# Kernel tuning notes

Measured on AMD Instinct MI355X. Metric: run time of the kernel, lower is better.

Reference implementation:

```python
import jax, jax.numpy as jnp
import numpy as np

# dims derived from config (hidden=512, d_state=64, d_conv=4, expand=2, headdim=64, ngroups=1)
D_MODEL = 512
D_STATE = 64
D_CONV = 4
D_INNER = 2 * D_MODEL          # 1024
HEADDIM = 64
NHEADS = D_INNER // HEADDIM    # 16
CONV_DIM = D_INNER + 2 * D_STATE   # 1152
D_IN_PROJ = 2 * D_INNER + 2 * D_STATE + NHEADS  # 2192
B = 4
L_TOT = 1024                   # seq_len (1008) + puzzle_emb_len (16)
INTER_T = 2816                 # find_multiple(round(4*1024*2/3), 256)
INTER_M = 1536                 # find_multiple(round(4*512*2/3), 256)
EPS = 1e-5


def rms_norm(x, eps=EPS):
    # weightless RMSNorm computed in fp32 (as HRM's rms_norm)
    x32 = x.astype(jnp.float32)
    y = x32 * jax.lax.rsqrt(jnp.mean(x32 * x32, axis=-1, keepdims=True) + eps)
    return y.astype(x.dtype)


def silu(x):
    return x * jax.nn.sigmoid(x)


def swiglu(x, w_gu, w_d):
    gate, up = jnp.split(x @ w_gu.T, 2, axis=-1)
    return (silu(gate) * up) @ w_d.T


def mamba2(u, in_proj_w, conv_w, conv_b, dt_bias, A_log, D, norm_w, out_proj_w):
    b, l, _ = u.shape
    zxbcdt = u @ in_proj_w.T                       # (b, l, D_IN_PROJ)
    z = zxbcdt[..., :D_INNER]
    xBC = zxbcdt[..., D_INNER:D_INNER + CONV_DIM]
    dt = jax.nn.softplus(zxbcdt[..., -NHEADS:] + dt_bias)  # (b, l, H)
    # causal depthwise conv1d over time + SiLU
    xp = jnp.pad(xBC, ((0, 0), (D_CONV - 1, 0), (0, 0)))
    xc = conv_b + sum(xp[:, i:i + l, :] * conv_w[:, i] for i in range(D_CONV))
    xBC = silu(xc)
    x = xBC[..., :D_INNER].reshape(b, l, NHEADS, HEADDIM)      # (b,l,h,p)
    Bm = xBC[..., D_INNER:D_INNER + D_STATE]                    # (b,l,n) ngroups=1
    Cm = xBC[..., D_INNER + D_STATE:]                           # (b,l,n)
    A = -jnp.exp(A_log)                                         # (h,)

    def step(s, inp):
        x_t, B_t, C_t, dt_t = inp                # (b,h,p) (b,n) (b,n) (b,h)
        dA = jnp.exp(dt_t * A)                   # (b,h)
        s = s * dA[:, :, None, None] + (dt_t[:, :, None] * x_t)[..., None] * B_t[:, None, None, :]
        y_t = jnp.einsum('bhpn,bn->bhp', s, C_t)
        return s, y_t

    s0 = jnp.zeros((b, NHEADS, HEADDIM, D_STATE), u.dtype)
    xs = (x.transpose(1, 0, 2, 3), Bm.transpose(1, 0, 2), Cm.transpose(1, 0, 2), dt.transpose(1, 0, 2))
    _, ys = jax.lax.scan(step, s0, xs)
    y = ys.transpose(1, 0, 2, 3) + x * D[None, None, :, None]   # skip term D*x per head
    y = y.reshape(b, l, D_INNER)
    # gated RMSNorm (norm_before_gate=False): norm(y * silu(z)) * weight
    g = y * silu(z)
    g32 = g.astype(jnp.float32)
    g = (g32 * jax.lax.rsqrt(jnp.mean(g32 * g32, axis=-1, keepdims=True) + EPS)).astype(g.dtype) * norm_w
    return g @ out_proj_w.T


def setup_inputs() -> dict:
    key = jax.random.key(0)
    ks = jax.random.split(key, 12)
    s = 0.02
    return {
        'hidden_states': jax.random.normal(ks[0], (B, L_TOT, D_MODEL), jnp.float32),
        'in_proj_w': jax.random.normal(ks[1], (D_IN_PROJ, D_MODEL), jnp.float32) * s,
        'conv_w': jax.random.normal(ks[2], (CONV_DIM, D_CONV), jnp.float32) * 0.1,
        'conv_b': jnp.zeros((CONV_DIM,), jnp.float32),
        'dt_bias': jax.random.normal(ks[3], (NHEADS,), jnp.float32) * 0.5,
        'A_log': jnp.log(jnp.arange(1, NHEADS + 1, dtype=jnp.float32)),
        'D': jnp.ones((NHEADS,), jnp.float32),
        'norm_w': jnp.ones((D_INNER,), jnp.float32),
        'out_proj_w': jax.random.normal(ks[4], (D_MODEL, D_INNER), jnp.float32) * s,
        'gu_t': jax.random.normal(ks[5], (2 * INTER_T, L_TOT), jnp.float32) * s,
        'down_t': jax.random.normal(ks[6], (L_TOT, INTER_T), jnp.float32) * s,
        'gu_m': jax.random.normal(ks[7], (2 * INTER_M, D_MODEL), jnp.float32) * s,
        'down_m': jax.random.normal(ks[8], (D_MODEL, INTER_M), jnp.float32) * s,
    }


def reference(hidden_states, in_proj_w, conv_w, conv_b, dt_bias, A_log, D, norm_w, out_proj_w, gu_t, down_t, gu_m, down_m):
    # Mamba2 mixer -> post-norm
    h = rms_norm(hidden_states + mamba2(hidden_states, in_proj_w, conv_w, conv_b, dt_bias, A_log, D, norm_w, out_proj_w))
    # MLP-t cross mixer over the sequence dim -> post-norm
    x = h.transpose(0, 2, 1)                 # (b, d, L)
    x = rms_norm(x + swiglu(x, gu_t, down_t))
    h = x.transpose(0, 2, 1)
    # token MLP -> post-norm
    h = rms_norm(h + swiglu(h, gu_m, down_m))
    return h
```

## Files before the change

### kernel.cpp

```cpp
#include <hip/hip_runtime.h>


#define BB 4
#define LL 1024
#define DMODEL 512
#define DINNER 1024
#define NHEADS 16
#define HEADDIM 64
#define DSTATE 64
#define CONVDIM 1152
#define NPROJ 2192
#define NPROJ_PAD 2304
#define INTER_T 2816
#define INTER_M 1536
#define NCHUNK 32
#define CHUNK 32

typedef __bf16 bf16x8 __attribute__((ext_vector_type(8)));
typedef float  f32x4  __attribute__((ext_vector_type(4)));
typedef unsigned short u16;
typedef unsigned int   u32;

__device__ __forceinline__ u16 f2bf(float x) {
    union { float f; u32 u; } v; v.f = x;
    u32 u = v.u;
    return (u16)((u + 0x7fffu + ((u >> 16) & 1u)) >> 16);
}
__device__ __forceinline__ float silu_f(float x) {
    return x / (1.f + __expf(-x));
}
__device__ __forceinline__ float bf2f(u16 w) {
    union { u32 u; float f; } a; a.u = ((u32)w) << 16; return a.f;
}

__device__ __forceinline__ void gld_lds16(const u16* g, u16* l) {
    __builtin_amdgcn_global_load_lds(
        (const __attribute__((address_space(1))) unsigned int*)g,
        (__attribute__((address_space(3))) unsigned int*)l, 16, 0, 0);
}

__device__ __forceinline__ float block_sum(float v) {
    #pragma unroll
    for (int off = 32; off > 0; off >>= 1) v += __shfl_xor(v, off, 64);
    __shared__ float red[4];
    int w = threadIdx.x >> 6;
    int nwv = blockDim.x >> 6;
    if ((threadIdx.x & 63) == 0) red[w] = v;
    __syncthreads();
    float tot = red[0];
    for (int i = 1; i < nwv; i++) tot += red[i];
    return tot;
}

#define HID_E      2097152LL
#define INPROJ_P_E 1179648LL
#define INPROJ_S_E 1122304LL
#define OUTPROJ_E   524288LL
#define GUT_E      5767168LL
#define DOWNT_E    2883584LL
#define GUM_E      1572864LL
#define DOWNM_E     786432LL
#define CONV_TOT_E 14811136LL

__global__ __launch_bounds__(256) void convert_all_kernel(
    const float* __restrict__ s_hid, const float* __restrict__ s_inproj,
    const float* __restrict__ s_outproj, const float* __restrict__ s_gut,
    const float* __restrict__ s_downt, const float* __restrict__ s_gum,
    const float* __restrict__ s_downm, u16* __restrict__ dst)
{
    long long idx = (long long)blockIdx.x * 256 + threadIdx.x;
    long long e = idx * 4;
    if (e >= CONV_TOT_E) return;
    const float* src; long long off, nsrc;
    long long c0 = HID_E;
    long long c1 = c0 + INPROJ_P_E;
    long long c2 = c1 + OUTPROJ_E;
    long long c3 = c2 + GUT_E;
    long long c4 = c3 + DOWNT_E;
    long long c5 = c4 + GUM_E;
    if      (e < c0) { src = s_hid;     off = e;      nsrc = HID_E; }
    else if (e < c1) { src = s_inproj;  off = e - c0; nsrc = INPROJ_S_E; }
    else if (e < c2) { src = s_outproj; off = e - c1; nsrc = OUTPROJ_E; }
    else if (e < c3) { src = s_gut;     off = e - c2; nsrc = GUT_E; }
    else if (e < c4) { src = s_downt;   off = e - c3; nsrc = DOWNT_E; }
    else if (e < c5) { src = s_gum;     off = e - c4; nsrc = GUM_E; }
    else             { src = s_downm;   off = e - c5; nsrc = DOWNM_E; }
    ushort4 r;
    if (off < nsrc) {
        float4 v = *reinterpret_cast<const float4*>(src + off);
        r.x = f2bf(v.x); r.y = f2bf(v.y); r.z = f2bf(v.z); r.w = f2bf(v.w);
    } else {
        r.x = 0; r.y = 0; r.z = 0; r.w = 0;
    }
    *reinterpret_cast<ushort4*>(dst + e) = r;
}

template<bool SK>
__device__ __forceinline__ void gemm_bt_body(
    const u16* __restrict__ A, const u16* __restrict__ W,
    float* __restrict__ C, int M, int N, int K, int kLen)
{
    __shared__ u16 As[128 * 64];
    __shared__ u16 Bs[128 * 64];
    int tid = threadIdx.x;
    int m0 = blockIdx.y * 128, n0 = blockIdx.x * 128;
    int kBase = SK ? blockIdx.z * kLen : 0;
    float* Cw = SK ? C + (size_t)blockIdx.z * M * N : C;
    int wave = tid >> 6, lane = tid & 63;
    int wm = (wave >> 1) * 64, wn = (wave & 1) * 64;
    int lrow = lane & 15;
    int kq = lane >> 4;
    int kx = lrow & 7;

    int rL = lane >> 3, cL = lane & 7;
    int cG = cL ^ rL;
    const u16* gA[4]; const u16* gB[4];
    u16 *lA[4], *lB[4];
    #pragma unroll
    for (int i = 0; i < 4; i++) {
        int r = wave * 32 + i * 8;
        gA[i] = A + (size_t)(m0 + r + rL) * K + kBase + cG * 8;
        gB[i] = W + (size_t)(n0 + r + rL) * K + kBase + cG * 8;
        lA[i] = &As[r * 64];
        lB[i] = &Bs[r * 64];
    }

    f32x4 acc[4][4];
    #pragma unroll
    for (int i = 0; i < 4; i++)
        #pragma unroll
        for (int j = 0; j < 4; j++) {
            acc[i][j][0] = 0.f; acc[i][j][1] = 0.f;
            acc[i][j][2] = 0.f; acc[i][j][3] = 0.f;
        }

    for (int kt = 0; kt < kLen; kt += 64) {
        __syncthreads();
        #pragma unroll
        for (int i = 0; i < 4; i++) {
            gld_lds16(gA[i] + kt, lA[i]);
            gld_lds16(gB[i] + kt, lB[i]);
        }
        __syncthreads();
        #pragma unroll
        for (int ks = 0; ks < 2; ks++) {
            int ko = (((ks * 4 + kq) ^ kx) * 8);
            bf16x8 af[4], bfr[4];
            #pragma unroll
            for (int i = 0; i < 4; i++) {
                af[i]  = *reinterpret_cast<const bf16x8*>(&As[(wm + i * 16 + lrow) * 64 + ko]);
                bfr[i] = *reinterpret_cast<const bf16x8*>(&Bs[(wn + i * 16 + lrow) * 64 + ko]);
            }
            #pragma unroll
            for (int i = 0; i < 4; i++)
                #pragma unroll
                for (int j = 0; j < 4; j++)
                    acc[i][j] = __builtin_amdgcn_mfma_f32_16x16x32_bf16(af[i], bfr[j], acc[i][j], 0, 0, 0);
        }
    }

    int rbase = m0 + wm + kq * 4;
    int cbase = n0 + wn + lrow;
    #pragma unroll
    for (int i = 0; i < 4; i++)
        #pragma unroll
        for (int j = 0; j < 4; j++)
            #pragma unroll
            for (int r = 0; r < 4; r++)
                Cw[(size_t)(rbase + i * 16 + r) * N + cbase + j * 16] = acc[i][j][r];
}

__global__ __launch_bounds__(256) void gemm_bt(
    const u16* __restrict__ A, const u16* __restrict__ W,
    float* __restrict__ C, int M, int N, int K)
{
    gemm_bt_body<false>(A, W, C, M, N, K, K);
}

__global__ __launch_bounds__(256) void gemm_bt_sk(
    const u16* __restrict__ A, const u16* __restrict__ W,
    float* __restrict__ C, int M, int N, int K, int kLen)
{
    gemm_bt_body<true>(A, W, C, M, N, K, kLen);
}

__global__ __launch_bounds__(256) void gemm_swiglu(
    const u16* __restrict__ A, const u16* __restrict__ W,
    u16* __restrict__ act, int M, int inter, int K)
{
    __shared__ u16 As[128 * 64];
    __shared__ u16 Bs[128 * 64];
    int tid = threadIdx.x;
    int m0 = blockIdx.y * 128, n0 = blockIdx.x * 64;
    int wave = tid >> 6, lane = tid & 63;
    int wm = (wave >> 1) * 64, wn = (wave & 1) * 32;
    int lrow = lane & 15;
    int kq = lane >> 4;
    int kx = lrow & 7;

    int rL = lane >> 3, cL = lane & 7;
    int cG = cL ^ rL;
    const u16* gA[4]; const u16* gB[4];
    u16 *lA[4], *lB[4];
    #pragma unroll
    for (int i = 0; i < 4; i++) {
        int r = wave * 32 + i * 8;
        gA[i] = A + (size_t)(m0 + r + rL) * K + cG * 8;
        lA[i] = &As[r * 64];
        int rB = r;
        int grow = (rB < 64) ? (n0 + rB + rL)
                             : (inter + n0 + rB - 64 + rL);
        gB[i] = W + (size_t)grow * K + cG * 8;
        lB[i] = &Bs[rB * 64];
    }

    f32x4 accg[4][2], accu[4][2];
    #pragma unroll
    for (int i = 0; i < 4; i++)
        #pragma unroll
        for (int j = 0; j < 2; j++) {
            accg[i][j][0]=0.f; accg[i][j][1]=0.f; accg[i][j][2]=0.f; accg[i][j][3]=0.f;
            accu[i][j][0]=0.f; accu[i][j][1]=0.f; accu[i][j][2]=0.f; accu[i][j][3]=0.f;
        }

    for (int kt = 0; kt < K; kt += 64) {
        __syncthreads();
        #pragma unroll
        for (int i = 0; i < 4; i++) {
            gld_lds16(gA[i] + kt, lA[i]);
            gld_lds16(gB[i] + kt, lB[i]);
        }
        __syncthreads();
        #pragma unroll
        for (int ks = 0; ks < 2; ks++) {
            int ko = (((ks * 4 + kq) ^ kx) * 8);
            bf16x8 af[4], bg[2], bu[2];
            #pragma unroll
            for (int i = 0; i < 4; i++)
                af[i] = *reinterpret_cast<const bf16x8*>(&As[(wm + i * 16 + lrow) * 64 + ko]);
            #pragma unroll
            for (int j = 0; j < 2; j++) {
                bg[j] = *reinterpret_cast<const bf16x8*>(&Bs[(wn + j * 16 + lrow) * 64 + ko]);
                bu[j] = *reinterpret_cast<const bf16x8*>(&Bs[(64 + wn + j * 16 + lrow) * 64 + ko]);
            }
            #pragma unroll
            for (int i = 0; i < 4; i++)
                #pragma unroll
                for (int j = 0; j < 2; j++) {
                    accg[i][j] = __builtin_amdgcn_mfma_f32_16x16x32_bf16(af[i], bg[j], accg[i][j], 0, 0, 0);
                    accu[i][j] = __builtin_amdgcn_mfma_f32_16x16x32_bf16(af[i], bu[j], accu[i][j], 0, 0, 0);
                }
        }
    }

    int rbase = m0 + wm + kq * 4;
    int cbase = n0 + wn + lrow;
    #pragma unroll
    for (int i = 0; i < 4; i++)
        #pragma unroll
        for (int j = 0; j < 2; j++)
            #pragma unroll
            for (int r = 0; r < 4; r++) {
                float g = accg[i][j][r], u = accu[i][j][r];
                act[(size_t)(rbase + i * 16 + r) * inter + cbase + j * 16] =
                    f2bf(silu_f(g) * u);
            }
}

__global__ __launch_bounds__(256) void conv_dt_kernel(
    const float* __restrict__ zx, const float* __restrict__ conv_w,
    const float* __restrict__ conv_b, const float* __restrict__ dt_bias,
    float* __restrict__ convout, float* __restrict__ dtbuf)
{
    int idx = blockIdx.x * 256 + threadIdx.x;
    int bl = idx / 1168;
    int c  = idx - bl * 1168;
    int l  = bl & (LL - 1);
    if (c < CONVDIM) {
        const float* col = zx + (size_t)bl * NPROJ_PAD + DINNER + c;
        float acc = conv_b[c];
        #pragma unroll
        for (int i = 0; i < 4; i++) {
            int lt = l - 3 + i;
            float v = (lt >= 0) ? col[(long long)(lt - l) * NPROJ_PAD] : 0.f;
            acc = fmaf(v, conv_w[c * 4 + i], acc);
        }
        convout[(size_t)bl * CONVDIM + c] = silu_f(acc);
    } else {
        int h = c - CONVDIM;
        float v = zx[(size_t)bl * NPROJ_PAD + 2176 + h] + dt_bias[h];
        float sp = (v > 20.f) ? v : log1pf(__expf(v));
        dtbuf[(size_t)bl * NHEADS + h] = sp;
    }
}

__global__ __launch_bounds__(256) void scan_mfma1(
    const float* __restrict__ convout, const float* __restrict__ dtbuf,
    const float* __restrict__ A_log, float* __restrict__ Sc,
    float* __restrict__ Ptot, float* __restrict__ yp0)
{
    __shared__ u16 Blds[32 * 72];
    __shared__ u16 Clds[32 * 72];
    __shared__ u16 Xt[4][64 * 40];
    __shared__ u16 Bht[4][64 * 40];
    __shared__ u16 Wlds[4][32 * 40];
    __shared__ float dtl[4][32], cuml[4][32], warr[4][32];

    int blk = blockIdx.x;
    int c   = blk & 31;
    int bg  = blk >> 5;
    int b   = bg >> 2;
    int hq  = bg & 3;
    int tid = threadIdx.x;
    int w    = tid >> 6;
    int lane = tid & 63;
    int h   = hq * 4 + w;
    int bh  = b * 16 + h;
    int lrow = lane & 15, kq = lane >> 4;
    size_t base = ((size_t)b * LL + (size_t)c * CHUNK) * CONVDIM;
    float Ah = -__expf(A_log[h]);

    if (lane < 32)
        dtl[w][lane] = dtbuf[((size_t)b * LL + (size_t)c * CHUNK + lane) * NHEADS + h];
    #pragma unroll
    for (int it = 0; it < 4; ++it) {
        int idx = it * 256 + tid;
        int t = idx >> 5, q = idx & 31;
        float4 v = *reinterpret_cast<const float4*>(
            &convout[base + (size_t)t * CONVDIM + DINNER + q * 4]);
        ushort4 r4; r4.x = f2bf(v.x); r4.y = f2bf(v.y); r4.z = f2bf(v.z); r4.w = f2bf(v.w);
        if (q < 16) *reinterpret_cast<ushort4*>(&Blds[t * 72 + q * 4]) = r4;
        else        *reinterpret_cast<ushort4*>(&Clds[t * 72 + (q - 16) * 4]) = r4;
    }
    #pragma unroll
    for (int t = 0; t < 32; ++t) {
        float v = convout[base + (size_t)t * CONVDIM + h * HEADDIM + lane];
        Xt[w][lane * 40 + t] = f2bf(v);
    }
    __syncthreads();

    float s_inc = 0.f, s_all = 0.f;
    #pragma unroll
    for (int j = 0; j < 32; ++j) {
        float v = dtl[w][j];
        s_all += v;
        if (j <= lane) s_inc += v;
    }
    if (lane < 32) {
        cuml[w][lane] = s_inc;
        warr[w][lane] = __expf(Ah * (s_all - s_inc)) * dtl[w][lane];
    }
    float cumTot = s_all;
    __syncthreads();

    #pragma unroll
    for (int t = 0; t < 32; ++t)
        Bht[w][lane * 40 + t] = f2bf(warr[w][t] * bf2f(Blds[t * 72 + lane]));

    f32x4 accG[2][2];
    #pragma unroll
    for (int i = 0; i < 2; i++)
        #pragma unroll
        for (int j = 0; j < 2; j++) {
            accG[i][j][0]=0.f; accG[i][j][1]=0.f; accG[i][j][2]=0.f; accG[i][j][3]=0.f;
        }
    #pragma unroll
    for (int ks = 0; ks < 2; ++ks) {
        bf16x8 af[2], bfr[2];
        #pragma unroll
        for (int i = 0; i < 2; i++) {
            af[i]  = *reinterpret_cast<const bf16x8*>(&Clds[(16*i + lrow) * 72 + ks*32 + kq*8]);
            bfr[i] = *reinterpret_cast<const bf16x8*>(&Blds[(16*i + lrow) * 72 + ks*32 + kq*8]);
        }
        #pragma unroll
        for (int i = 0; i < 2; i++)
            #pragma unroll
            for (int j = 0; j < 2; j++)
                accG[i][j] = __builtin_amdgcn_mfma_f32_16x16x32_bf16(af[i], bfr[j], accG[i][j], 0, 0, 0);
    }

    float ctp0 = cuml[w][lrow],      dtp0 = dtl[w][lrow];
    float ctp1 = cuml[w][16 + lrow], dtp1 = dtl[w][16 + lrow];
    #pragma unroll
    for (int i = 0; i < 2; i++)
        #pragma unroll
        for (int r = 0; r < 4; r++) {
            int t = 16*i + kq*4 + r;
            float ct = cuml[w][t];
            #pragma unroll
            for (int j = 0; j < 2; j++) {
                int tp = 16*j + lrow;
                float ctp = j ? ctp1 : ctp0;
                float dtp = j ? dtp1 : dtp0;
                float g = accG[i][j][r];
                float wv = (tp <= t) ? __expf(Ah * (ct - ctp)) * dtp * g : 0.f;
                Wlds[w][t * 40 + tp] = f2bf(wv);
            }
        }
    __syncthreads();

    bf16x8 xf[4];
    #pragma unroll
    for (int j = 0; j < 4; j++)
        xf[j] = *reinterpret_cast<const bf16x8*>(&Xt[w][(16*j + lrow) * 40 + kq*8]);
    f32x4 accY[2][4];
    #pragma unroll
    for (int i = 0; i < 2; i++) {
        bf16x8 wf = *reinterpret_cast<const bf16x8*>(&Wlds[w][(16*i + lrow) * 40 + kq*8]);
        #pragma unroll
        for (int j = 0; j < 4; j++) {
            accY[i][j][0]=0.f; accY[i][j][1]=0.f; accY[i][j][2]=0.f; accY[i][j][3]=0.f;
            accY[i][j] = __builtin_amdgcn_mfma_f32_16x16x32_bf16(wf, xf[j], accY[i][j], 0, 0, 0);
        }
    }

    f32x4 accS[4][4];
    #pragma unroll
    for (int j = 0; j < 4; j++) {
        bf16x8 bb = *reinterpret_cast<const bf16x8*>(&Bht[w][(16*j + lrow) * 40 + kq*8]);
        #pragma unroll
        for (int i = 0; i < 4; i++) {
            accS[i][j][0]=0.f; accS[i][j][1]=0.f; accS[i][j][2]=0.f; accS[i][j][3]=0.f;
            accS[i][j] = __builtin_amdgcn_mfma_f32_16x16x32_bf16(xf[i], bb, accS[i][j], 0, 0, 0);
        }
    }

    float* yb = yp0 + ((size_t)b * LL + (size_t)c * CHUNK) * DINNER + h * HEADDIM;
    #pragma unroll
    for (int i = 0; i < 2; i++)
        #pragma unroll
        for (int r = 0; r < 4; r++) {
            int t = 16*i + kq*4 + r;
            #pragma unroll
            for (int j = 0; j < 4; j++)
                yb[(size_t)t * DINNER + 16*j + lrow] = accY[i][j][r];
        }
    #pragma unroll
    for (int i = 0; i < 4; i++)
        #pragma unroll
        for (int r = 0; r < 4; r++) {
            int p = 16*i + kq*4 + r;
            #pragma unroll
            for (int j = 0; j < 4; j++)
                Sc[((size_t)(bh * 4 + j) * NCHUNK + c) * 1024 + p * 16 + lrow] = accS[i][j][r];
        }
    if (lane == 0) Ptot[bh * NCHUNK + c] = __expf(Ah * cumTot);
}

__global__ __launch_bounds__(256) void scan_combine(
    const float* __restrict__ Sc, const float* __restrict__ Ptot,
    float* __restrict__ Sinit)
{
    int blk = blockIdx.x;
    int bh = blk >> 2;
    int tid = threadIdx.x;
    int p = tid >> 2;
    int ncol = (tid & 3) * 4;
    float4 carry; carry.x = 0.f; carry.y = 0.f; carry.z = 0.f; carry.w = 0.f;
    for (int c = 0; c < NCHUNK; ++c) {
        size_t row = ((size_t)blk * NCHUNK + c) * 1024 + p * 16 + ncol;
        *reinterpret_cast<float4*>(Sinit + row) = carry;
        float P = Ptot[bh * NCHUNK + c];
        float4 si = *reinterpret_cast<const float4*>(Sc + row);
        carry.x = fmaf(carry.x, P, si.x);
        carry.y = fmaf(carry.y, P, si.y);
        carry.z = fmaf(carry.z, P, si.z);
        carry.w = fmaf(carry.w, P, si.w);
    }
}

__global__ __launch_bounds__(64) void scan_mfma2(
    const float* __restrict__ convout, const float* __restrict__ dtbuf,
    const float* __restrict__ A_log, const float* __restrict__ Sinit,
    float* __restrict__ yp1)
{
    __shared__ u16 Clds2[32 * 72];
    __shared__ float dtl[32], dacl[32];
    int blk = blockIdx.x;
    int c   = blk & 31;
    int bh  = blk >> 5;
    int b = bh >> 4, h = bh & 15;
    int lane = threadIdx.x;
    int lrow = lane & 15, kq = lane >> 4;
    size_t base = ((size_t)b * LL + (size_t)c * CHUNK) * CONVDIM;
    float Ah = -__expf(A_log[h]);

    if (lane < 32)
        dtl[lane] = dtbuf[((size_t)b * LL + (size_t)c * CHUNK + lane) * NHEADS + h];
    __syncthreads();
    float s_inc = 0.f;
    #pragma unroll
    for (int j = 0; j < 32; ++j) {
        float v = dtl[j];
        if (j <= lane) s_inc += v;
    }
    if (lane < 32) dacl[lane] = __expf(Ah * s_inc);
    __syncthreads();
    #pragma unroll
    for (int it = 0; it < 8; ++it) {
        int idx = it * 64 + lane;
        int t = idx >> 4, q = idx & 15;
        float sc = dacl[t];
        float4 v = *reinterpret_cast<const float4*>(
            &convout[base + (size_t)t * CONVDIM + DINNER + DSTATE + q * 4]);
        ushort4 r4;
        r4.x = f2bf(v.x * sc); r4.y = f2bf(v.y * sc);
        r4.z = f2bf(v.z * sc); r4.w = f2bf(v.w * sc);
        *reinterpret_cast<ushort4*>(&Clds2[t * 72 + q * 4]) = r4;
    }
    __syncthreads();

    f32x4 accI[2][4];
    #pragma unroll
    for (int i = 0; i < 2; i++)
        #pragma unroll
        for (int j = 0; j < 4; j++) {
            accI[i][j][0]=0.f; accI[i][j][1]=0.f; accI[i][j][2]=0.f; accI[i][j][3]=0.f;
        }
    #pragma unroll
    for (int ks = 0; ks < 2; ++ks) {
        bf16x8 ca[2];
        #pragma unroll
        for (int i = 0; i < 2; i++)
            ca[i] = *reinterpret_cast<const bf16x8*>(&Clds2[(16*i + lrow) * 72 + ks*32 + kq*8]);
        int nq = ks * 2 + (kq >> 1);
        int off = (kq & 1) * 8;
        #pragma unroll
        for (int j = 0; j < 4; j++) {
            int p = 16*j + lrow;
            const float* sp = Sinit + ((size_t)(bh * 4 + nq) * NCHUNK + c) * 1024 + p * 16 + off;
            float4 a = *reinterpret_cast<const float4*>(sp);
            float4 b4 = *reinterpret_cast<const float4*>(sp + 4);
            union { u16 us[8]; bf16x8 v; } fr;
            fr.us[0] = f2bf(a.x);  fr.us[1] = f2bf(a.y);
            fr.us[2] = f2bf(a.z);  fr.us[3] = f2bf(a.w);
            fr.us[4] = f2bf(b4.x); fr.us[5] = f2bf(b4.y);
            fr.us[6] = f2bf(b4.z); fr.us[7] = f2bf(b4.w);
            #pragma unroll
            for (int i = 0; i < 2; i++)
                accI[i][j] = __builtin_amdgcn_mfma_f32_16x16x32_bf16(ca[i], fr.v, accI[i][j], 0, 0, 0);
        }
    }

    float* yb = yp1 + ((size_t)b * LL + (size_t)c * CHUNK) * DINNER + h * HEADDIM;
    #pragma unroll
    for (int i = 0; i < 2; i++)
        #pragma unroll
        for (int r = 0; r < 4; r++) {
            int t = 16*i + kq*4 + r;
            #pragma unroll
            for (int j = 0; j < 4; j++)
                yb[(size_t)t * DINNER + 16*j + lrow] = accI[i][j][r];
        }
}

__global__ __launch_bounds__(256) void gated_rms_kernel(
    const float* __restrict__ yp0, const float* __restrict__ yp1,
    const float* __restrict__ convout, const float* __restrict__ zx,
    const float* __restrict__ Dv, const float* __restrict__ norm_w,
    u16* __restrict__ gout)
{
    int bl = blockIdx.x;
    int c = threadIdx.x * 4;
    float4 y0 = *reinterpret_cast<const float4*>(yp0 + (size_t)bl * DINNER + c);
    float4 y1 = *reinterpret_cast<const float4*>(yp1 + (size_t)bl * DINNER + c);
    float4 xv = *reinterpret_cast<const float4*>(convout + (size_t)bl * CONVDIM + c);
    float4 zv = *reinterpret_cast<const float4*>(zx + (size_t)bl * NPROJ_PAD + c);
    float Dh = Dv[c >> 6];
    float g0 = (y0.x + y1.x + xv.x * Dh) * silu_f(zv.x);
    float g1 = (y0.y + y1.y + xv.y * Dh) * silu_f(zv.y);
    float g2 = (y0.z + y1.z + xv.z * Dh) * silu_f(zv.z);
    float g3 = (y0.w + y1.w + xv.w * Dh) * silu_f(zv.w);
    float tot = block_sum(g0 * g0 + g1 * g1 + g2 * g2 + g3 * g3);
    float sc = rsqrtf(tot * (1.f / DINNER) + 1e-5f);
    float4 nw = *reinterpret_cast<const float4*>(norm_w + c);
    ushort4 o;
    o.x = f2bf(g0 * sc * nw.x); o.y = f2bf(g1 * sc * nw.y);
    o.z = f2bf(g2 * sc * nw.z); o.w = f2bf(g3 * sc * nw.w);
    *reinterpret_cast<ushort4*>(gout + (size_t)bl * DINNER + c) = o;
}

__global__ void residual_rms_sk_kernel(
    const float* __restrict__ a, const float* __restrict__ pbuf,
    float* __restrict__ outf, int ncols, int rows)
{
    int row = blockIdx.x;
    int c = threadIdx.x * 4;
    size_t slice = (size_t)rows * ncols;
    size_t off = (size_t)row * ncols + c;
    float4 va = *reinterpret_cast<const float4*>(a + off);
    float4 p0 = *reinterpret_cast<const float4*>(pbuf + off);
    float4 p1 = *reinterpret_cast<const float4*>(pbuf + slice + off);
    float4 p2 = *reinterpret_cast<const float4*>(pbuf + 2 * slice + off);
    float4 p3 = *reinterpret_cast<const float4*>(pbuf + 3 * slice + off);
    float v0 = va.x + ((p0.x + p1.x) + (p2.x + p3.x));
    float v1 = va.y + ((p0.y + p1.y) + (p2.y + p3.y));
    float v2 = va.z + ((p0.z + p1.z) + (p2.z + p3.z));
    float v3 = va.w + ((p0.w + p1.w) + (p2.w + p3.w));
    float tot = block_sum(v0 * v0 + v1 * v1 + v2 * v2 + v3 * v3);
    float sc = rsqrtf(tot / (float)ncols + 1e-5f);
    float4 o; o.x = v0 * sc; o.y = v1 * sc; o.z = v2 * sc; o.w = v3 * sc;
    *reinterpret_cast<float4*>(outf + off) = o;
}

__global__ __launch_bounds__(256) void transpose_dual_kernel(
    const float* __restrict__ in, u16* __restrict__ outb,
    float* __restrict__ outf, int R, int C)
{
    __shared__ float tile[32][33];
    int b = blockIdx.z;
    int c0 = blockIdx.x * 32, r0 = blockIdx.y * 32;
    const float* ip = in + (size_t)b * R * C;
    for (int i = threadIdx.y; i < 32; i += 8)
        tile[i][threadIdx.x] = ip[(size_t)(r0 + i) * C + c0 + threadIdx.x];
    __syncthreads();
    size_t ob = (size_t)b * R * C;
    for (int i = threadIdx.y; i < 32; i += 8) {
        float v = tile[threadIdx.x][i];
        size_t oi = ob + (size_t)(c0 + i) * R + r0 + threadIdx.x;
        outf[oi] = v;
        outb[oi] = f2bf(v);
    }
}

extern "C" void kernel_launch(void* const* d_in, const int* in_sizes, int n_in,
                              void* d_out, int out_size, void* d_ws, size_t ws_size,
                              hipStream_t stream)
{
    const float* hid      = (const float*)d_in[0];
    const float* in_proj  = (const float*)d_in[1];
    const float* conv_w   = (const float*)d_in[2];
    const float* conv_b   = (const float*)d_in[3];
    const float* dt_bias  = (const float*)d_in[4];
    const float* A_log    = (const float*)d_in[5];
    const float* Dv       = (const float*)d_in[6];
    const float* norm_w   = (const float*)d_in[7];
    const float* out_proj = (const float*)d_in[8];
    const float* gu_t     = (const float*)d_in[9];
    const float* down_t   = (const float*)d_in[10];
    const float* gu_m     = (const float*)d_in[11];
    const float* down_m   = (const float*)d_in[12];
    float* outp = (float*)d_out;

    char* ws = (char*)d_ws;
    u16* bf        = (u16*)ws;
    u16* hid_bf    = bf;
    u16* w_inproj  = bf + HID_E;
    u16* w_outproj = w_inproj + INPROJ_P_E;
    u16* w_gut     = w_outproj + OUTPROJ_E;
    u16* w_downt   = w_gut + GUT_E;
    u16* w_gum     = w_downt + DOWNT_E;
    u16* w_downm   = w_gum + GUM_E;
    size_t o = (size_t)(CONV_TOT_E * 2);
    auto alloc = [&](size_t bytes) { size_t r = o; o = (o + bytes + 255) & ~(size_t)255; return r; };
    size_t dt_off  = alloc(4096 * 16 * 4);
    size_t g_off   = alloc((size_t)4096 * 1024 * 2);
    size_t h1_off  = alloc((size_t)4096 * 512 * 4);
    size_t Pt_off  = alloc(2048 * 4);
    size_t xtb_off = alloc((size_t)2048 * 1024 * 2);
    size_t xtf_off = alloc((size_t)2048 * 1024 * 4);
    size_t act1_off= alloc((size_t)2048 * 2816 * 2);
    size_t x2_off  = alloc((size_t)2048 * 1024 * 4);
    size_t h2b_off = alloc((size_t)4096 * 512 * 2);
    size_t h2f_off = alloc((size_t)4096 * 512 * 4);
    size_t act2_off= alloc((size_t)4096 * 1536 * 2);
    size_t pad_off = alloc((size_t)10 * 1024 * 1024);
    size_t Sc_off  = xtb_off;
    size_t Si_off  = xtb_off + (size_t)8192 * 1024 * 4;
    (void)pad_off;
    size_t R_off   = o;
    size_t zx_off  = R_off;
    size_t cv_off  = zx_off + (size_t)4096 * NPROJ_PAD * 4;
    size_t y_off   = cv_off + (size_t)4096 * CONVDIM * 4;
    size_t sk_off  = R_off;

    float* zx      = (float*)(ws + zx_off);
    float* convout = (float*)(ws + cv_off);
    float* ybuf    = (float*)(ws + y_off);
    float* dtbuf   = (float*)(ws + dt_off);
    u16*   g_bf    = (u16*)(ws + g_off);
    float* h1      = (float*)(ws + h1_off);
    u16*   xt_bf   = (u16*)(ws + xtb_off);
    float* xt_f    = (float*)(ws + xtf_off);
    u16*   act1    = (u16*)(ws + act1_off);
    float* x2      = (float*)(ws + x2_off);
    u16*   h2_bf   = (u16*)(ws + h2b_off);
    float* h2_f    = (float*)(ws + h2f_off);
    u16*   act2    = (u16*)(ws + act2_off);
    float* skbuf   = (float*)(ws + sk_off);
    float* Sc      = (float*)(ws + Sc_off);
    float* Sinit   = (float*)(ws + Si_off);
    float* Ptot    = (float*)(ws + Pt_off);

    convert_all_kernel<<<14464, 256, 0, stream>>>(
        hid, in_proj, out_proj, gu_t, down_t, gu_m, down_m, bf);

    gemm_bt<<<dim3(NPROJ_PAD / 128, 4096 / 128), 256, 0, stream>>>(
        hid_bf, w_inproj, zx, 4096, NPROJ_PAD, 512);

    conv_dt_kernel<<<18688, 256, 0, stream>>>(zx, conv_w, conv_b, dt_bias, convout, dtbuf);

    scan_mfma1<<<512, 256, 0, stream>>>(convout, dtbuf, A_log, Sc, Ptot, ybuf);
    scan_combine<<<256, 256, 0, stream>>>(Sc, Ptot, Sinit);
    scan_mfma2<<<2048, 64, 0, stream>>>(convout, dtbuf, A_log, Sinit, Sc);

    gated_rms_kernel<<<4096, 256, 0, stream>>>(ybuf, Sc, convout, zx, Dv, norm_w, g_bf);

    gemm_bt_sk<<<dim3(512 / 128, 4096 / 128, 4), 256, 0, stream>>>(
        g_bf, w_outproj, skbuf, 4096, 512, 1024, 256);

    residual_rms_sk_kernel<<<4096, 128, 0, stream>>>(hid, skbuf, h1, 512, 4096);

    transpose_dual_kernel<<<dim3(16, 32, 4), dim3(32, 8), 0, stream>>>(h1, xt_bf, xt_f, 1024, 512);

    gemm_swiglu<<<dim3(INTER_T / 64, 2048 / 128), 256, 0, stream>>>(
        xt_bf, w_gut, act1, 2048, INTER_T, 1024);

    gemm_bt_sk<<<dim3(1024 / 128, 2048 / 128, 4), 256, 0, stream>>>(
        act1, w_downt, skbuf, 2048, 1024, 2816, 704);

    residual_rms_sk_kernel<<<2048, 256, 0, stream>>>(xt_f, skbuf, x2, 1024, 2048);

    transpose_dual_kernel<<<dim3(32, 16, 4), dim3(32, 8), 0, stream>>>(x2, h2_bf, h2_f, 512, 1024);

    gemm_swiglu<<<dim3(INTER_M / 64, 4096 / 128), 256, 0, stream>>>(
        h2_bf, w_gum, act2, 4096, INTER_M, 512);

    gemm_bt_sk<<<dim3(512 / 128, 4096 / 128, 4), 256, 0, stream>>>(
        act2, w_downm, skbuf, 4096, 512, 1536, 384);

    residual_rms_sk_kernel<<<4096, 128, 0, stream>>>(h2_f, skbuf, outp, 512, 4096);
}
```

Measured before the change: 341.4 us.

## Share C tile across four heads in scan_mfma2; preload chunk decays in combine

scan_mfma2 now runs four heads per 256-thread block, one wave per head. All four waves share a single bf16 copy of the chunk's C tile in LDS, so the C load and conversion is done once instead of once per head. The per-timestep decay factor is now applied to the output rows instead of to C, which is algebraically equivalent because it is a per-row scale. scan_combine loads all chunk decay factors into registers up front and unrolls the chunk loop, taking the scalar loads off the sequential carry chain. The cost is more registers in the combine kernel and a fourfold smaller grid for scan_mfma2.

```diff
diff --git a/kernel.cpp b/kernel.cpp
--- a/kernel.cpp
+++ b/kernel.cpp
@@ -456,59 +456,66 @@
     int tid = threadIdx.x;
     int p = tid >> 2;
     int ncol = (tid & 3) * 4;
+    float Pv[NCHUNK];
+    #pragma unroll
+    for (int c = 0; c < NCHUNK; ++c) Pv[c] = Ptot[bh * NCHUNK + c];
     float4 carry; carry.x = 0.f; carry.y = 0.f; carry.z = 0.f; carry.w = 0.f;
+    size_t rowbase = (size_t)blk * NCHUNK * 1024 + p * 16 + ncol;
+    #pragma unroll
     for (int c = 0; c < NCHUNK; ++c) {
-        size_t row = ((size_t)blk * NCHUNK + c) * 1024 + p * 16 + ncol;
+        size_t row = rowbase + (size_t)c * 1024;
         *reinterpret_cast<float4*>(Sinit + row) = carry;
-        float P = Ptot[bh * NCHUNK + c];
         float4 si = *reinterpret_cast<const float4*>(Sc + row);
-        carry.x = fmaf(carry.x, P, si.x);
-        carry.y = fmaf(carry.y, P, si.y);
-        carry.z = fmaf(carry.z, P, si.z);
-        carry.w = fmaf(carry.w, P, si.w);
-    }
-}
-
-__global__ __launch_bounds__(64) void scan_mfma2(
+        carry.x = fmaf(carry.x, Pv[c], si.x);
+        carry.y = fmaf(carry.y, Pv[c], si.y);
+        carry.z = fmaf(carry.z, Pv[c], si.z);
+        carry.w = fmaf(carry.w, Pv[c], si.w);
+    }
+}
+
+__global__ __launch_bounds__(256) void scan_mfma2(
     const float* __restrict__ convout, const float* __restrict__ dtbuf,
     const float* __restrict__ A_log, const float* __restrict__ Sinit,
     float* __restrict__ yp1)
 {
     __shared__ u16 Clds2[32 * 72];
-    __shared__ float dtl[32], dacl[32];
+    __shared__ float dtl[4][32], dacl[4][32];
     int blk = blockIdx.x;
     int c   = blk & 31;
-    int bh  = blk >> 5;
-    int b = bh >> 4, h = bh & 15;
-    int lane = threadIdx.x;
+    int bg  = blk >> 5;
+    int b   = bg >> 2;
+    int hq  = bg & 3;
+    int tid = threadIdx.x;
+    int w    = tid >> 6;
+    int lane = tid & 63;
+    int h   = hq * 4 + w;
+    int bh  = b * 16 + h;
     int lrow = lane & 15, kq = lane >> 4;
     size_t base = ((size_t)b * LL + (size_t)c * CHUNK) * CONVDIM;
     float Ah = -__expf(A_log[h]);
 
     if (lane < 32)
-        dtl[lane] = dtbuf[((size_t)b * LL + (size_t)c * CHUNK + lane) * NHEADS + h];
-    __syncthreads();
-    float s_inc = 0.f;
-    #pragma unroll
-    for (int j = 0; j < 32; ++j) {
-        float v = dtl[j];
-        if (j <= lane) s_inc += v;
-    }
-    if (lane < 32) dacl[lane] = __expf(Ah * s_inc);
-    __syncthreads();
-    #pragma unroll
-    for (int it = 0; it < 8; ++it) {
-        int idx = it * 64 + lane;
+        dtl[w][lane] = dtbuf[((size_t)b * LL + (size_t)c * CHUNK + lane) * NHEADS + h];
+    #pragma unroll
+    for (int it = 0; it < 2; ++it) {
+        int idx = it * 256 + tid;
         int t = idx >> 4, q = idx & 15;
-        float sc = dacl[t];
         float4 v = *reinterpret_cast<const float4*>(
             &convout[base + (size_t)t * CONVDIM + DINNER + DSTATE + q * 4]);
         ushort4 r4;
-        r4.x = f2bf(v.x * sc); r4.y = f2bf(v.y * sc);
-        r4.z = f2bf(v.z * sc); r4.w = f2bf(v.w * sc);
+        r4.x = f2bf(v.x); r4.y = f2bf(v.y);
+        r4.z = f2bf(v.z); r4.w = f2bf(v.w);
         *reinterpret_cast<ushort4*>(&Clds2[t * 72 + q * 4]) = r4;
     }
     __syncthreads();
+
+    float s_inc = 0.f;
+    #pragma unroll
+    for (int j = 0; j < 32; ++j) {
+        float v = dtl[w][j];
+        if (j <= lane) s_inc += v;
+    }
+    if (lane < 32) dacl[w][lane] = __expf(Ah * s_inc);
 
     f32x4 accI[2][4];
     #pragma unroll
@@ -548,9 +555,10 @@
         #pragma unroll
         for (int r = 0; r < 4; r++) {
             int t = 16*i + kq*4 + r;
+            float sct = dacl[w][t];
             #pragma unroll
             for (int j = 0; j < 4; j++)
-                yb[(size_t)t * DINNER + 16*j + lrow] = accI[i][j][r];
+                yb[(size_t)t * DINNER + 16*j + lrow] = accI[i][j][r] * sct;
         }
 }
 
@@ -702,7 +710,7 @@
 
     scan_mfma1<<<512, 256, 0, stream>>>(convout, dtbuf, A_log, Sc, Ptot, ybuf);
     scan_combine<<<256, 256, 0, stream>>>(Sc, Ptot, Sinit);
-    scan_mfma2<<<2048, 64, 0, stream>>>(convout, dtbuf, A_log, Sinit, Sc);
+    scan_mfma2<<<512, 256, 0, stream>>>(convout, dtbuf, A_log, Sinit, Sc);
 
     gated_rms_kernel<<<4096, 256, 0, stream>>>(ybuf, Sc, convout, zx, Dv, norm_w, g_bf);
 
```

New measurement: 345.6 us. Within noise of the previous version (+1.2%).
